# Kernel tuning notes

Hardware: AMD Instinct MI355X
Metric: run time of the kernel (lower is better)

The kernel has to match this reference:

```python
import jax, jax.numpy as jnp
import numpy as np

B, N, IN_DIM, OUT_DIM = 8, 2048, 128, 128


def setup_inputs() -> dict:
    key = jax.random.key(0)
    k_a, k_h, k_wp, k_bp, k_wa, k_ba = jax.random.split(key, 6)
    a = jax.random.uniform(k_a, (B, N, N), dtype=jnp.float32)
    h = jax.random.normal(k_h, (B, N, IN_DIM), dtype=jnp.float32)
    # nn.Linear(in_dim, out_dim): y = x @ W^T + b ; store W already transposed.
    W_proj = jax.random.normal(k_wp, (IN_DIM, OUT_DIM), dtype=jnp.float32) / np.sqrt(IN_DIM)
    b_proj = jax.random.normal(k_bp, (OUT_DIM,), dtype=jnp.float32) * 0.01
    # nn.Linear(2*out_dim, 1): weight vector of length 2*out_dim + scalar bias.
    w_att = jax.random.normal(k_wa, (2 * OUT_DIM,), dtype=jnp.float32) / np.sqrt(2 * OUT_DIM)
    b_att = jax.random.normal(k_ba, (), dtype=jnp.float32) * 0.01
    return {"a": a, "h": h, "W_proj": W_proj, "b_proj": b_proj,
            "w_att": w_att, "b_att": b_att}


def reference(a, h, W_proj, b_proj, w_att, b_att):
    # h: [B, N, in_dim] -> [B, N, out_dim]
    h = h @ W_proj + b_proj
    d = w_att.shape[0] // 2
    # GAT decomposition: attention(cat(h_i, h_j)) = h_i.w_src + h_j.w_dst + b
    # (identical math to expand+cat+Linear, without the O(B*N^2*2D) tensor)
    s = h @ w_att[:d]            # [B, N] contribution of row node i
    t = h @ w_att[d:]            # [B, N] contribution of col node j
    e = jax.nn.relu(s[:, :, None] + t[:, None, :] + b_att)  # [B, N, N]
    att = jnp.exp(e) * a
    att = att / jnp.sum(att, axis=-1, keepdims=True)
    return att @ h + h           # [B, N, out_dim]
```

## Files before the change

### kernel.cpp

```cpp
#include <hip/hip_runtime.h>
#include <hip/hip_bf16.h>

#define NB 8
#define NN 2048
#define DD 128
#define WST 36

__device__ __forceinline__ void gll16(const void* g, void* l) {
    __builtin_amdgcn_global_load_lds(
        (const __attribute__((address_space(1))) void*)g,
        (__attribute__((address_space(3))) void*)l, 16, 0, 0);
}

__global__ __launch_bounds__(256) void proj_kernel(
    const float* __restrict__ h, const float* __restrict__ W,
    const float* __restrict__ bias, const float* __restrict__ watt,
    float* __restrict__ hp, float* __restrict__ s, float* __restrict__ t)
{
    __shared__ float Ws[64][132];
    __shared__ float hs[64][68];
    const int tid = threadIdx.x;
    const int rowbase = blockIdx.x * 64;
    const int rg = tid >> 3;
    const int dg = tid & 7;

    const float4* W4 = (const float4*)W;
    const float4* h4 = (const float4*)h;

    float acc[2][16];
    #pragma unroll
    for (int r = 0; r < 2; ++r)
        #pragma unroll
        for (int d = 0; d < 16; ++d) acc[r][d] = 0.f;

    for (int p = 0; p < 2; ++p) {
        #pragma unroll
        for (int q = 0; q < 8; ++q) {
            int f = tid + 256 * q;
            float4 v = W4[2048 * p + f];
            *(float4*)&Ws[f >> 5][4 * (f & 31)] = v;
        }
        #pragma unroll
        for (int q = 0; q < 4; ++q) {
            int f = tid + 256 * q;
            int r = f >> 4, c4 = f & 15;
            float4 v = h4[(size_t)(rowbase + r) * 32 + 16 * p + c4];
            *(float4*)&hs[r][4 * c4] = v;
        }
        __syncthreads();

        #pragma unroll 8
        for (int k = 0; k < 64; ++k) {
            float h0 = hs[2 * rg][k];
            float h1 = hs[2 * rg + 1][k];
            float4 w0 = *(const float4*)&Ws[k][dg * 16];
            float4 w1 = *(const float4*)&Ws[k][dg * 16 + 4];
            float4 w2 = *(const float4*)&Ws[k][dg * 16 + 8];
            float4 w3 = *(const float4*)&Ws[k][dg * 16 + 12];
            float wv[16] = {w0.x,w0.y,w0.z,w0.w, w1.x,w1.y,w1.z,w1.w,
                            w2.x,w2.y,w2.z,w2.w, w3.x,w3.y,w3.z,w3.w};
            #pragma unroll
            for (int d = 0; d < 16; ++d) {
                acc[0][d] += h0 * wv[d];
                acc[1][d] += h1 * wv[d];
            }
        }
        __syncthreads();
    }

    const float4* b4 = (const float4*)bias;
    #pragma unroll
    for (int dq = 0; dq < 4; ++dq) {
        float4 bv = b4[dg * 4 + dq];
        #pragma unroll
        for (int r = 0; r < 2; ++r) {
            acc[r][4 * dq + 0] += bv.x;
            acc[r][4 * dq + 1] += bv.y;
            acc[r][4 * dq + 2] += bv.z;
            acc[r][4 * dq + 3] += bv.w;
        }
    }
    #pragma unroll
    for (int r = 0; r < 2; ++r) {
        float4* o = (float4*)(hp + (size_t)(rowbase + 2 * rg + r) * 128);
        #pragma unroll
        for (int dq = 0; dq < 4; ++dq) {
            float4 v = {acc[r][4*dq+0], acc[r][4*dq+1], acc[r][4*dq+2], acc[r][4*dq+3]};
            o[dg * 4 + dq] = v;
        }
    }
    const float4* w4 = (const float4*)watt;
    float sp[2] = {0.f, 0.f}, tp[2] = {0.f, 0.f};
    #pragma unroll
    for (int q = 0; q < 4; ++q) {
        float4 wsa = w4[dg * 4 + q];
        float4 wta = w4[32 + dg * 4 + q];
        #pragma unroll
        for (int r = 0; r < 2; ++r) {
            sp[r] += acc[r][4*q+0]*wsa.x + acc[r][4*q+1]*wsa.y
                   + acc[r][4*q+2]*wsa.z + acc[r][4*q+3]*wsa.w;
            tp[r] += acc[r][4*q+0]*wta.x + acc[r][4*q+1]*wta.y
                   + acc[r][4*q+2]*wta.z + acc[r][4*q+3]*wta.w;
        }
    }
    #pragma unroll
    for (int r = 0; r < 2; ++r) {
        float v = sp[r], u = tp[r];
        v += __shfl_xor(v, 1, 64); u += __shfl_xor(u, 1, 64);
        v += __shfl_xor(v, 2, 64); u += __shfl_xor(u, 2, 64);
        v += __shfl_xor(v, 4, 64); u += __shfl_xor(u, 4, 64);
        if (dg == 0) {
            s[rowbase + 2 * rg + r] = v;
            t[rowbase + 2 * rg + r] = u;
        }
    }
}

__global__ __launch_bounds__(256, 2) void fused_kernel(
    const float* __restrict__ a, const float* __restrict__ hp,
    const float* __restrict__ s, const float* __restrict__ t,
    const float* __restrict__ battp, float* __restrict__ out)
{
    __shared__ float hp_s[2][32][128];
    __shared__ float w_s[2][32][WST];
    __shared__ float wsum_s[32];

    const int tid  = threadIdx.x;
    const int lane = tid & 63;
    const int wid  = tid >> 6;
    const int b     = blockIdx.x >> 6;
    const int ibase = (blockIdx.x & 63) * 32;
    const int bN    = b * NN;

    const int jqA  = tid & 7;
    const int rowA = tid >> 3;
    const int dg   = tid & 15;
    const int rg8  = ((tid >> 4) & 3) * 8;
    const int jh   = wid;

    const float batt = battp[0];
    const float4* a4  = (const float4*)a;
    const float4* t4  = (const float4*)t;
    const float4* hp4 = (const float4*)hp;
    float4* out4 = (float4*)out;

    const float s_reg = s[bN + ibase + rowA];
    const size_t arow = (size_t)(bN + ibase + rowA) * 512;

    float wsum_p = 0.f;
    float acc[8][8];
    #pragma unroll
    for (int r = 0; r < 8; ++r)
        #pragma unroll
        for (int d = 0; d < 8; ++d) acc[r][d] = 0.f;

    float4 a_nx, t_nx;

#define LOADA(tt) do { \
        a_nx = a4[arow + (tt) * 8 + jqA]; \
        t_nx = t4[(bN >> 2) + (tt) * 8 + jqA]; \
    } while (0)

#define GLL(tt, nb) do { \
        const float* gsrc = hp + (size_t)(bN + (tt) * 32) * 128 + wid * 1024 + lane * 4; \
        float* ldst = &hp_s[nb][0][0] + wid * 1024; \
        gll16(gsrc,       ldst); \
        gll16(gsrc + 256, ldst + 256); \
        gll16(gsrc + 512, ldst + 512); \
        gll16(gsrc + 768, ldst + 768); \
    } while (0)

#define PHASEA(nb) do { \
        float av[4] = {a_nx.x, a_nx.y, a_nx.z, a_nx.w}; \
        float tv[4] = {t_nx.x, t_nx.y, t_nx.z, t_nx.w}; \
        _Pragma("unroll") \
        for (int k = 0; k < 4; ++k) { \
            float e = fmaxf(s_reg + tv[k] + batt, 0.f); \
            float p = __expf(e) * av[k]; \
            wsum_p += p; \
            w_s[nb][4 * jqA + k][rowA] = p; \
        } \
    } while (0)

#define PHASEB(cb) do { \
        _Pragma("unroll") \
        for (int jj = 0; jj < 8; ++jj) { \
            int j = jh * 8 + jj; \
            float4 wa = *(const float4*)&w_s[cb][j][rg8]; \
            float4 wb = *(const float4*)&w_s[cb][j][rg8 + 4]; \
            float4 ha = *(const float4*)&hp_s[cb][j][4 * dg]; \
            float4 hb = *(const float4*)&hp_s[cb][j][64 + 4 * dg]; \
            float wv[8] = {wa.x,wa.y,wa.z,wa.w, wb.x,wb.y,wb.z,wb.w}; \
            float hv[8] = {ha.x,ha.y,ha.z,ha.w, hb.x,hb.y,hb.z,hb.w}; \
            _Pragma("unroll") \
            for (int r = 0; r < 8; ++r) \
                _Pragma("unroll") \
                for (int d = 0; d < 8; ++d) \
                    acc[r][d] += wv[r] * hv[d]; \
        } \
    } while (0)

    GLL(0, 0);
    LOADA(0);
    PHASEA(0);
    LOADA(1);
    __syncthreads();

    int cur = 0;
    for (int tt = 0; tt < 64; ++tt) {
        if (tt < 63) {
            GLL(tt + 1, cur ^ 1);
            PHASEA(cur ^ 1);
            if (tt < 62) LOADA(tt + 2);
        }
        PHASEB(cur);
        __syncthreads();
        cur ^= 1;
    }

    {
        float v = wsum_p;
        v += __shfl_xor(v, 1, 64);
        v += __shfl_xor(v, 2, 64);
        v += __shfl_xor(v, 4, 64);
        if (jqA == 0) wsum_s[rowA] = v;
    }

    float (*red)[32][128] = (float (*)[32][128])hp_s;
    if (jh >= 2) {
        #pragma unroll
        for (int r = 0; r < 8; ++r) {
            float4 v0 = {acc[r][0], acc[r][1], acc[r][2], acc[r][3]};
            float4 v1 = {acc[r][4], acc[r][5], acc[r][6], acc[r][7]};
            *(float4*)&red[jh - 2][rg8 + r][4 * dg]      = v0;
            *(float4*)&red[jh - 2][rg8 + r][64 + 4 * dg] = v1;
        }
    }
    __syncthreads();
    if (jh < 2) {
        #pragma unroll
        for (int r = 0; r < 8; ++r) {
            float4 v0 = *(const float4*)&red[jh][rg8 + r][4 * dg];
            float4 v1 = *(const float4*)&red[jh][rg8 + r][64 + 4 * dg];
            acc[r][0] += v0.x; acc[r][1] += v0.y; acc[r][2] += v0.z; acc[r][3] += v0.w;
            acc[r][4] += v1.x; acc[r][5] += v1.y; acc[r][6] += v1.z; acc[r][7] += v1.w;
        }
    }
    __syncthreads();
    if (jh == 1) {
        #pragma unroll
        for (int r = 0; r < 8; ++r) {
            float4 v0 = {acc[r][0], acc[r][1], acc[r][2], acc[r][3]};
            float4 v1 = {acc[r][4], acc[r][5], acc[r][6], acc[r][7]};
            *(float4*)&red[0][rg8 + r][4 * dg]      = v0;
            *(float4*)&red[0][rg8 + r][64 + 4 * dg] = v1;
        }
    }
    __syncthreads();
    if (jh == 0) {
        #pragma unroll
        for (int r = 0; r < 8; ++r) {
            int row = rg8 + r;
            float inv = 1.0f / wsum_s[row];
            size_t gr = (size_t)(bN + ibase + row);
            float4 r0 = *(const float4*)&red[0][row][4 * dg];
            float4 r1 = *(const float4*)&red[0][row][64 + 4 * dg];
            float4 h0 = hp4[gr * 32 + dg];
            float4 h1 = hp4[gr * 32 + 16 + dg];
            float4 o0, o1;
            o0.x = (acc[r][0] + r0.x) * inv + h0.x;
            o0.y = (acc[r][1] + r0.y) * inv + h0.y;
            o0.z = (acc[r][2] + r0.z) * inv + h0.z;
            o0.w = (acc[r][3] + r0.w) * inv + h0.w;
            o1.x = (acc[r][4] + r1.x) * inv + h1.x;
            o1.y = (acc[r][5] + r1.y) * inv + h1.y;
            o1.z = (acc[r][6] + r1.z) * inv + h1.z;
            o1.w = (acc[r][7] + r1.w) * inv + h1.w;
            out4[gr * 32 + dg]      = o0;
            out4[gr * 32 + 16 + dg] = o1;
        }
    }
}

extern "C" void kernel_launch(void* const* d_in, const int* in_sizes, int n_in,
                              void* d_out, int out_size, void* d_ws, size_t ws_size,
                              hipStream_t stream) {
    const float* a      = (const float*)d_in[0];
    const float* h      = (const float*)d_in[1];
    const float* W_proj = (const float*)d_in[2];
    const float* b_proj = (const float*)d_in[3];
    const float* w_att  = (const float*)d_in[4];
    const float* b_att  = (const float*)d_in[5];
    float* out = (float*)d_out;

    float* hp = (float*)d_ws;
    float* s  = hp + (size_t)NB * NN * DD;
    float* t  = s + (size_t)NB * NN;

    proj_kernel<<<256, 256, 0, stream>>>(h, W_proj, b_proj, w_att, hp, s, t);
    fused_kernel<<<512, 256, 0, stream>>>(a, hp, s, t, b_att, out);
}
```

Measured before the change: 307.6 us.

## Use bf16 MFMA for attention-weighted aggregation with transposed bf16 features

```diff
diff --git a/kernel.cpp b/kernel.cpp
--- a/kernel.cpp
+++ b/kernel.cpp
@@ -4,18 +4,22 @@
 #define NB 8
 #define NN 2048
 #define DD 128
-#define WST 36
-
-__device__ __forceinline__ void gll16(const void* g, void* l) {
-    __builtin_amdgcn_global_load_lds(
-        (const __attribute__((address_space(1))) void*)g,
-        (__attribute__((address_space(3))) void*)l, 16, 0, 0);
+#define NT 32
+
+typedef __attribute__((ext_vector_type(8))) short short8v;
+typedef __attribute__((ext_vector_type(4))) float f32x4;
+
+__device__ __forceinline__ unsigned short f2bf(float x) {
+    unsigned int u = __float_as_uint(x);
+    u += 0x7FFFu + ((u >> 16) & 1u);
+    return (unsigned short)(u >> 16);
 }
 
 __global__ __launch_bounds__(256) void proj_kernel(
     const float* __restrict__ h, const float* __restrict__ W,
     const float* __restrict__ bias, const float* __restrict__ watt,
-    float* __restrict__ hp, float* __restrict__ s, float* __restrict__ t)
+    float* __restrict__ hp, unsigned short* __restrict__ hpT,
+    float* __restrict__ s, float* __restrict__ t)
 {
     __shared__ float Ws[64][132];
     __shared__ float hs[64][68];
@@ -89,6 +93,18 @@
             o[dg * 4 + dq] = v;
         }
     }
+    {
+        int rowpair = ((rowbase & (NN - 1)) >> 1) + rg;
+        int bb = rowbase >> 11;
+        unsigned int* hT32 = (unsigned int*)hpT;
+        #pragma unroll
+        for (int dd = 0; dd < 16; ++dd) {
+            int d = dg * 16 + dd;
+            unsigned int pk = (unsigned int)f2bf(acc[0][dd]) |
+                              ((unsigned int)f2bf(acc[1][dd]) << 16);
+            hT32[(((size_t)bb * 128 + d) << 10) + rowpair] = pk;
+        }
+    }
     const float4* w4 = (const float4*)watt;
     float sp[2] = {0.f, 0.f}, tp[2] = {0.f, 0.f};
     #pragma unroll
@@ -116,104 +132,106 @@
     }
 }
 
-__global__ __launch_bounds__(256, 2) void fused_kernel(
+__global__ __launch_bounds__(256, 4) void fused_kernel(
     const float* __restrict__ a, const float* __restrict__ hp,
+    const unsigned short* __restrict__ hpT,
     const float* __restrict__ s, const float* __restrict__ t,
     const float* __restrict__ battp, float* __restrict__ out)
 {
-    __shared__ float hp_s[2][32][128];
-    __shared__ float w_s[2][32][WST];
-    __shared__ float wsum_s[32];
+    __shared__ unsigned short hpT_s[2][128 * 64];
+    __shared__ unsigned short w_s[2][16 * 64];
+    __shared__ float wsum_s[16];
 
     const int tid  = threadIdx.x;
     const int lane = tid & 63;
-    const int wid  = tid >> 6;
-    const int b     = blockIdx.x >> 6;
-    const int ibase = (blockIdx.x & 63) * 32;
+    const int wv   = tid >> 6;
+    const int b     = blockIdx.x >> 7;
+    const int ibase = (blockIdx.x & 127) * 16;
     const int bN    = b * NN;
 
-    const int jqA  = tid & 7;
-    const int rowA = tid >> 3;
-    const int dg   = tid & 15;
-    const int rg8  = ((tid >> 4) & 3) * 8;
-    const int jh   = wid;
+    const int rowA = tid >> 4;
+    const int q    = tid & 15;
+    const int sd   = tid >> 1;
+    const int sj   = (tid & 1) * 64;
 
     const float batt = battp[0];
-    const float4* a4  = (const float4*)a;
-    const float4* t4  = (const float4*)t;
-    const float4* hp4 = (const float4*)hp;
-    float4* out4 = (float4*)out;
-
+    const float4* a4 = (const float4*)a;
+    const float4* t4 = (const float4*)t;
     const float s_reg = s[bN + ibase + rowA];
     const size_t arow = (size_t)(bN + ibase + rowA) * 512;
+    const unsigned short* hTg = hpT + (((size_t)(b * 128 + sd)) << 11) + (tid & 1) * 32;
 
     float wsum_p = 0.f;
-    float acc[8][8];
-    #pragma unroll
-    for (int r = 0; r < 8; ++r)
-        #pragma unroll
-        for (int d = 0; d < 8; ++d) acc[r][d] = 0.f;
+    f32x4 acc0 = {0.f, 0.f, 0.f, 0.f};
+    f32x4 acc1 = {0.f, 0.f, 0.f, 0.f};
 
     float4 a_nx, t_nx;
+    uint4 hv0, hv1, hv2, hv3;
 
 #define LOADA(tt) do { \
-        a_nx = a4[arow + (tt) * 8 + jqA]; \
-        t_nx = t4[(bN >> 2) + (tt) * 8 + jqA]; \
-    } while (0)
-
-#define GLL(tt, nb) do { \
-        const float* gsrc = hp + (size_t)(bN + (tt) * 32) * 128 + wid * 1024 + lane * 4; \
-        float* ldst = &hp_s[nb][0][0] + wid * 1024; \
-        gll16(gsrc,       ldst); \
-        gll16(gsrc + 256, ldst + 256); \
-        gll16(gsrc + 512, ldst + 512); \
-        gll16(gsrc + 768, ldst + 768); \
+        a_nx = a4[arow + (tt) * 16 + q]; \
+        t_nx = t4[(bN >> 2) + (tt) * 16 + q]; \
+    } while (0)
+
+#define STAGELOAD(tt) do { \
+        const unsigned short* gp = hTg + (tt) * 64; \
+        hv0 = *(const uint4*)(gp);      hv1 = *(const uint4*)(gp + 8); \
+        hv2 = *(const uint4*)(gp + 16); hv3 = *(const uint4*)(gp + 24); \
+    } while (0)
+
+#define STAGEWRITE(nb) do { \
+        char* lb = (char*)hpT_s[nb]; \
+        int swz = (sd & 7) << 4; \
+        int bo = (sd << 7) + sj; \
+        *(uint4*)(lb + ((bo     ) ^ swz)) = hv0; \
+        *(uint4*)(lb + ((bo + 16) ^ swz)) = hv1; \
+        *(uint4*)(lb + ((bo + 32) ^ swz)) = hv2; \
+        *(uint4*)(lb + ((bo + 48) ^ swz)) = hv3; \
     } while (0)
 
 #define PHASEA(nb) do { \
-        float av[4] = {a_nx.x, a_nx.y, a_nx.z, a_nx.w}; \
-        float tv[4] = {t_nx.x, t_nx.y, t_nx.z, t_nx.w}; \
-        _Pragma("unroll") \
-        for (int k = 0; k < 4; ++k) { \
-            float e = fmaxf(s_reg + tv[k] + batt, 0.f); \
-            float p = __expf(e) * av[k]; \
-            wsum_p += p; \
-            w_s[nb][4 * jqA + k][rowA] = p; \
-        } \
-    } while (0)
-
-#define PHASEB(cb) do { \
-        _Pragma("unroll") \
-        for (int jj = 0; jj < 8; ++jj) { \
-            int j = jh * 8 + jj; \
-            float4 wa = *(const float4*)&w_s[cb][j][rg8]; \
-            float4 wb = *(const float4*)&w_s[cb][j][rg8 + 4]; \
-            float4 ha = *(const float4*)&hp_s[cb][j][4 * dg]; \
-            float4 hb = *(const float4*)&hp_s[cb][j][64 + 4 * dg]; \
-            float wv[8] = {wa.x,wa.y,wa.z,wa.w, wb.x,wb.y,wb.z,wb.w}; \
-            float hv[8] = {ha.x,ha.y,ha.z,ha.w, hb.x,hb.y,hb.z,hb.w}; \
-            _Pragma("unroll") \
-            for (int r = 0; r < 8; ++r) \
-                _Pragma("unroll") \
-                for (int d = 0; d < 8; ++d) \
-                    acc[r][d] += wv[r] * hv[d]; \
-        } \
-    } while (0)
-
-    GLL(0, 0);
+        float p0 = __expf(fmaxf(s_reg + t_nx.x + batt, 0.f)) * a_nx.x; \
+        float p1 = __expf(fmaxf(s_reg + t_nx.y + batt, 0.f)) * a_nx.y; \
+        float p2 = __expf(fmaxf(s_reg + t_nx.z + batt, 0.f)) * a_nx.z; \
+        float p3 = __expf(fmaxf(s_reg + t_nx.w + batt, 0.f)) * a_nx.w; \
+        wsum_p += (p0 + p1) + (p2 + p3); \
+        unsigned int u0 = (unsigned int)f2bf(p0) | ((unsigned int)f2bf(p1) << 16); \
+        unsigned int u1 = (unsigned int)f2bf(p2) | ((unsigned int)f2bf(p3) << 16); \
+        uint2 uu; uu.x = u0; uu.y = u1; \
+        *(uint2*)((char*)w_s[nb] + (((rowA << 7) + (q << 3)) ^ ((rowA & 7) << 4))) = uu; \
+    } while (0)
+
+#define DOMFMA(cb) do { \
+        const char* wb = (const char*)w_s[cb]; \
+        const char* hb = (const char*)hpT_s[cb]; \
+        int r = lane & 15; \
+        int kb = (lane >> 4) << 4; \
+        int swz = (r & 7) << 4; \
+        short8v A0 = *(const short8v*)(wb + (((r << 7) + kb     ) ^ swz)); \
+        short8v A1 = *(const short8v*)(wb + (((r << 7) + kb + 64) ^ swz)); \
+        int d0 = (wv << 5) + r; \
+        short8v B00 = *(const short8v*)(hb + (((d0 << 7) + kb     ) ^ swz)); \
+        short8v B01 = *(const short8v*)(hb + (((d0 << 7) + kb + 64) ^ swz)); \
+        short8v B10 = *(const short8v*)(hb + ((((d0 + 16) << 7) + kb     ) ^ swz)); \
+        short8v B11 = *(const short8v*)(hb + ((((d0 + 16) << 7) + kb + 64) ^ swz)); \
+        acc0 = __builtin_amdgcn_mfma_f32_16x16x32_bf16(A0, B00, acc0, 0, 0, 0); \
+        acc1 = __builtin_amdgcn_mfma_f32_16x16x32_bf16(A0, B10, acc1, 0, 0, 0); \
+        acc0 = __builtin_amdgcn_mfma_f32_16x16x32_bf16(A1, B01, acc0, 0, 0, 0); \
+        acc1 = __builtin_amdgcn_mfma_f32_16x16x32_bf16(A1, B11, acc1, 0, 0, 0); \
+    } while (0)
+
     LOADA(0);
+    STAGELOAD(0);
     PHASEA(0);
-    LOADA(1);
+    STAGEWRITE(0);
     __syncthreads();
 
     int cur = 0;
-    for (int tt = 0; tt < 64; ++tt) {
-        if (tt < 63) {
-            GLL(tt + 1, cur ^ 1);
-            PHASEA(cur ^ 1);
-            if (tt < 62) LOADA(tt + 2);
-        }
-        PHASEB(cur);
+    #pragma unroll 2
+    for (int tt = 0; tt < NT; ++tt) {
+        if (tt < NT - 1) { LOADA(tt + 1); STAGELOAD(tt + 1); }
+        DOMFMA(cur);
+        if (tt < NT - 1) { PHASEA(cur ^ 1); STAGEWRITE(cur ^ 1); }
         __syncthreads();
         cur ^= 1;
     }
@@ -223,63 +241,35 @@
         v += __shfl_xor(v, 1, 64);
         v += __shfl_xor(v, 2, 64);
         v += __shfl_xor(v, 4, 64);
-        if (jqA == 0) wsum_s[rowA] = v;
-    }
-
-    float (*red)[32][128] = (float (*)[32][128])hp_s;
-    if (jh >= 2) {
-        #pragma unroll
-        for (int r = 0; r < 8; ++r) {
-            float4 v0 = {acc[r][0], acc[r][1], acc[r][2], acc[r][3]};
-            float4 v1 = {acc[r][4], acc[r][5], acc[r][6], acc[r][7]};
-            *(float4*)&red[jh - 2][rg8 + r][4 * dg]      = v0;
-            *(float4*)&red[jh - 2][rg8 + r][64 + 4 * dg] = v1;
-        }
+        v += __shfl_xor(v, 8, 64);
+        if (q == 0) wsum_s[rowA] = v;
     }
     __syncthreads();
-    if (jh < 2) {
-        #pragma unroll
-        for (int r = 0; r < 8; ++r) {
-            float4 v0 = *(const float4*)&red[jh][rg8 + r][4 * dg];
-            float4 v1 = *(const float4*)&red[jh][rg8 + r][64 + 4 * dg];
-            acc[r][0] += v0.x; acc[r][1] += v0.y; acc[r][2] += v0.z; acc[r][3] += v0.w;
-            acc[r][4] += v1.x; acc[r][5] += v1.y; acc[r][6] += v1.z; acc[r][7] += v1.w;
-        }
-    }
-    __syncthreads();
-    if (jh == 1) {
-        #pragma unroll
-        for (int r = 0; r < 8; ++r) {
-            float4 v0 = {acc[r][0], acc[r][1], acc[r][2], acc[r][3]};
-            float4 v1 = {acc[r][4], acc[r][5], acc[r][6], acc[r][7]};
-            *(float4*)&red[0][rg8 + r][4 * dg]      = v0;
-            *(float4*)&red[0][rg8 + r][64 + 4 * dg] = v1;
-        }
-    }
-    __syncthreads();
-    if (jh == 0) {
-        #pragma unroll
-        for (int r = 0; r < 8; ++r) {
-            int row = rg8 + r;
-            float inv = 1.0f / wsum_s[row];
-            size_t gr = (size_t)(bN + ibase + row);
-            float4 r0 = *(const float4*)&red[0][row][4 * dg];
-            float4 r1 = *(const float4*)&red[0][row][64 + 4 * dg];
-            float4 h0 = hp4[gr * 32 + dg];
-            float4 h1 = hp4[gr * 32 + 16 + dg];
-            float4 o0, o1;
-            o0.x = (acc[r][0] + r0.x) * inv + h0.x;
-            o0.y = (acc[r][1] + r0.y) * inv + h0.y;
-            o0.z = (acc[r][2] + r0.z) * inv + h0.z;
-            o0.w = (acc[r][3] + r0.w) * inv + h0.w;
-            o1.x = (acc[r][4] + r1.x) * inv + h1.x;
-            o1.y = (acc[r][5] + r1.y) * inv + h1.y;
-            o1.z = (acc[r][6] + r1.z) * inv + h1.z;
-            o1.w = (acc[r][7] + r1.w) * inv + h1.w;
-            out4[gr * 32 + dg]      = o0;
-            out4[gr * 32 + 16 + dg] = o1;
-        }
-    }
+
+    {
+        int r = lane & 15;
+        int rloc = (lane >> 4) << 2;
+        float inv0 = 1.0f / wsum_s[rloc + 0];
+        float inv1 = 1.0f / wsum_s[rloc + 1];
+        float inv2 = 1.0f / wsum_s[rloc + 2];
+        float inv3 = 1.0f / wsum_s[rloc + 3];
+        int d0 = (wv << 5) + r;
+        const float* hpb = hp + (size_t)(bN + ibase) * 128;
+        float* ob = out + (size_t)(bN + ibase) * 128;
+        ob[(rloc + 0) * 128 + d0]      = acc0.x * inv0 + hpb[(rloc + 0) * 128 + d0];
+        ob[(rloc + 1) * 128 + d0]      = acc0.y * inv1 + hpb[(rloc + 1) * 128 + d0];
+        ob[(rloc + 2) * 128 + d0]      = acc0.z * inv2 + hpb[(rloc + 2) * 128 + d0];
+        ob[(rloc + 3) * 128 + d0]      = acc0.w * inv3 + hpb[(rloc + 3) * 128 + d0];
+        ob[(rloc + 0) * 128 + d0 + 16] = acc1.x * inv0 + hpb[(rloc + 0) * 128 + d0 + 16];
+        ob[(rloc + 1) * 128 + d0 + 16] = acc1.y * inv1 + hpb[(rloc + 1) * 128 + d0 + 16];
+        ob[(rloc + 2) * 128 + d0 + 16] = acc1.z * inv2 + hpb[(rloc + 2) * 128 + d0 + 16];
+        ob[(rloc + 3) * 128 + d0 + 16] = acc1.w * inv3 + hpb[(rloc + 3) * 128 + d0 + 16];
+    }
+#undef LOADA
+#undef STAGELOAD
+#undef STAGEWRITE
+#undef PHASEA
+#undef DOMFMA
 }
 
 extern "C" void kernel_launch(void* const* d_in, const int* in_sizes, int n_in,
@@ -296,7 +286,8 @@
     float* hp = (float*)d_ws;
     float* s  = hp + (size_t)NB * NN * DD;
     float* t  = s + (size_t)NB * NN;
-
-    proj_kernel<<<256, 256, 0, stream>>>(h, W_proj, b_proj, w_att, hp, s, t);
-    fused_kernel<<<512, 256, 0, stream>>>(a, hp, s, t, b_att, out);
-}
+    unsigned short* hpT = (unsigned short*)(t + (size_t)NB * NN);
+
+    proj_kernel<<<256, 256, 0, stream>>>(h, W_proj, b_proj, w_att, hp, hpT, s, t);
+    fused_kernel<<<1024, 256, 0, stream>>>(a, hp, hpT, s, t, b_att, out);
+}
```

New measurement: 264.3 us. 14.1% less time.
